# Optimization experiments

Measured on AMD Instinct MI355X. Metric: run time of the kernel, lower is better.

## Reference

```python
import jax, jax.numpy as jnp
import numpy as np

# module hyperparams (match init_kwargs)
C, K, S, RATIO, GC = 64, 7, 2, 2, 16
G = C // GC                      # 4 groups
KK = K * K                       # 49
NS = int(RATIO * S)              # 4
NN = NS * NS                     # 16
PAD = (K - 1) // 2               # 3
C1_IN = G * (2 * K * GC + KK)    # 1092
C1_OUT = G * NN * KK // 10       # 313
C2_OUT = G * NN * KK             # 3136
EPS = 1e-5


def _unfold(x, k, s, p):
    # torch.nn.Unfold: patches ordered (C, ki, kj) channel-major
    B, Cc, H, W = x.shape
    xp = jnp.pad(x, ((0, 0), (0, 0), (p, p), (p, p)))
    Ho = (H + 2 * p - k) // s + 1
    Wo = (W + 2 * p - k) // s + 1
    rows = jnp.arange(Ho)[:, None] * s + jnp.arange(k)[None, :]      # (Ho,k)
    cols = jnp.arange(Wo)[:, None] * s + jnp.arange(k)[None, :]      # (Wo,k)
    pat = xp[:, :, rows[:, :, None, None], cols[None, None, :, :]]   # (B,C,Ho,k,Wo,k)
    return pat.transpose(0, 1, 3, 5, 2, 4)                            # (B,C,k,k,Ho,Wo)


def setup_inputs() -> dict:
    key = jax.random.key(0)
    ks = jax.random.split(key, 5)
    x = jax.random.normal(ks[0], (8, C, 64, 64), dtype=jnp.float32)
    w1 = jax.random.normal(ks[1], (C1_OUT, C1_IN), dtype=jnp.float32) * 0.02
    gamma = jnp.ones((C1_OUT,), dtype=jnp.float32)   # BN weight (constant_init 1)
    beta = jnp.zeros((C1_OUT,), dtype=jnp.float32)   # BN bias
    w2 = jax.random.normal(ks[2], (C2_OUT, C1_OUT), dtype=jnp.float32) * 0.02
    b2 = jnp.zeros((C2_OUT,), dtype=jnp.float32)
    return {"x": x, "w1": w1, "gamma": gamma, "beta": beta, "w2": w2, "b2": b2}


def reference(x, w1, gamma, beta, w2, b2):
    B, _, H, W = x.shape
    pat = _unfold(x, K, S, PAD)                          # (B,C,K,K,Ho,Wo)
    Ho, Wo = pat.shape[-2], pat.shape[-1]
    xg = pat.reshape(B, G, GC, K, K, Ho, Wo)
    # three axis-wise max pools -> per-pixel descriptor
    x1 = xg.max(axis=2).reshape(B, G * K * K, Ho, Wo)
    x2 = xg.max(axis=3).reshape(B, G * GC * K, Ho, Wo)
    x3 = xg.max(axis=4).reshape(B, G * GC * K, Ho, Wo)
    feat = jnp.concatenate([x1, x2, x3], axis=1)         # (B, C1_IN, Ho, Wo)
    # conv1: 1x1 conv (no bias) + BN (batch stats) + ReLU
    h = jnp.einsum('bchw,oc->bohw', feat, w1)
    mu = h.mean(axis=(0, 2, 3), keepdims=True)
    var = h.var(axis=(0, 2, 3), keepdims=True)
    h = gamma[None, :, None, None] * (h - mu) * jax.lax.rsqrt(var + EPS) + beta[None, :, None, None]
    h = jax.nn.relu(h)
    # conv2: 1x1 conv with bias
    h2 = jnp.einsum('bchw,oc->bohw', h, w2) + b2[None, :, None, None]
    wt = h2.reshape(B, G, KK, NN, Ho, Wo)
    wt = jax.nn.softmax(wt, axis=2)                      # softmax over kernel positions
    # softmax-weighted patch reduction (mean over k*k)
    xk = xg.reshape(B, G, GC, KK, Ho, Wo)
    out = jnp.einsum('bgckhw,bgknhw->bgcnhw', xk, wt) / KK
    out = out.reshape(B, C, NS, NS, Ho, Wo)
    out = out.transpose(0, 1, 4, 2, 5, 3).reshape(B, C, Ho * NS, Wo * NS)
    return out
```

## Files before the change

kernel.cpp:

```cpp
#include <hip/hip_runtime.h>

namespace {
constexpr int kB    = 8;
constexpr int kC    = 64;
constexpr int kH    = 64, kW = 64;
constexpr int kNP   = 8192;
constexpr int kC1In = 1092;
constexpr int kKP   = 1152;
constexpr int kC1Out= 313;
constexpr int kC2Out= 3136;
constexpr int kC1P  = 320;
constexpr int kRowS = 56;
constexpr int kPosS = 16 * kRowS + 8;
constexpr int kPreFeat = 2048;
constexpr int kPreW2   = 490;
constexpr int kPreW1   = 1440;
constexpr int kPreBlocks = kPreFeat + kPreW2 + kPreW1;
}

typedef __attribute__((ext_vector_type(8))) short bf16x8;
typedef __attribute__((ext_vector_type(8))) _Float16 f16x8;
typedef __attribute__((ext_vector_type(2))) _Float16 h16x2;
typedef __attribute__((ext_vector_type(4))) float f32x4;

__device__ __forceinline__ unsigned short f2bf(float f) {
    unsigned u = __float_as_uint(f);
    unsigned r = (u + 0x7fffu + ((u >> 16) & 1u)) >> 16;
    return (unsigned short)r;
}

__global__ __launch_bounds__(256) void k_pre(const float* __restrict__ x,
        const float* __restrict__ w1, const float* __restrict__ w2,
        unsigned short* __restrict__ feat_bf, unsigned short* __restrict__ w1s,
        bf16x8* __restrict__ w2t, float* __restrict__ stats) {
    __shared__ float xs[16 * 7 * 40];
    int tid = threadIdx.x;
    int bid = blockIdx.x;

    if (bid < kPreFeat) {
        int g = bid >> 9, pt = bid & 511;
        int p0 = pt * 16;
        int b = p0 >> 10, i = (p0 >> 5) & 31, j0 = p0 & 31;
        int y0 = 2 * i - 3, xbase = 2 * j0 - 3;
        const float* xb = x + ((size_t)(b * 64 + g * 16) << 12);

        for (int idx = tid; idx < 16 * 7 * 40; idx += 256) {
            int ch = idx / 280, r2 = idx - ch * 280;
            int row = r2 / 40, col = r2 - row * 40;
            int yy = y0 + row, xx = xbase + col;
            float v = 0.f;
            if ((unsigned)yy < 64u && (unsigned)xx < 64u)
                v = xb[(ch << 12) + (yy << 6) + xx];
            xs[idx] = v;
        }
        __syncthreads();

        for (int o = tid; o < 16 * 273; o += 256) {
            int pos = o / 273, c = o - pos * 273;
            float m = -INFINITY;
            int cg;
            if (c < 49) {
                int a = c / 7, bk = c - a * 7;
                int base = a * 40 + 2 * pos + bk;
                #pragma unroll
                for (int ch = 0; ch < 16; ++ch) m = fmaxf(m, xs[ch * 280 + base]);
                cg = g * 49 + c;
            } else if (c < 161) {
                int r = c - 49;
                int ch = r / 7, bk = r - ch * 7;
                int base = ch * 280 + 2 * pos + bk;
                #pragma unroll
                for (int a = 0; a < 7; ++a) m = fmaxf(m, xs[base + a * 40]);
                cg = 196 + g * 112 + r;
            } else {
                int r = c - 161;
                int ch = r / 7, a = r - ch * 7;
                int base = ch * 280 + a * 40 + 2 * pos;
                #pragma unroll
                for (int bk = 0; bk < 7; ++bk) m = fmaxf(m, xs[base + bk]);
                cg = 644 + g * 112 + r;
            }
            feat_bf[(size_t)(p0 + pos) * kKP + cg] = f2bf(m);
        }
        if (g == 3) {
            for (int idx = tid; idx < 16 * 60; idx += 256) {
                int pos = idx / 60, c = idx - pos * 60;
                feat_bf[(size_t)(p0 + pos) * kKP + 1092 + c] = 0;
            }
        }
    } else if (bid < kPreFeat + kPreW2) {
        int idx = (bid - kPreFeat) * 256 + tid;
        int lane = idx & 63;
        int t = (idx >> 6) % 10;
        int k = (idx / 640) % 49;
        int g = idx / 31360;
        int n = lane & 15, c0 = t * 32 + ((lane >> 4) << 3);
        int row = g * 784 + k * 16 + n;
        bf16x8 hi;
        #pragma unroll
        for (int e = 0; e < 8; ++e) {
            int c = c0 + e;
            float v = (c < kC1Out) ? w2[(size_t)row * kC1Out + c] : 0.f;
            hi[e] = (short)f2bf(v);
        }
        w2t[idx] = hi;
    } else {
        int idx = (bid - kPreFeat - kPreW2) * 256 + tid;
        if (idx < 640) stats[idx] = 0.f;
        int r = idx / kKP, c = idx - r * kKP;
        float v = (r < kC1Out && c < kC1In) ? w1[(size_t)r * kC1In + c] : 0.f;
        w1s[idx] = f2bf(v);
    }
}

__global__ __launch_bounds__(512) void k_gemm1(
        const unsigned short* __restrict__ feat_bf, const unsigned short* __restrict__ w1s,
        float* __restrict__ h, float* __restrict__ sum_, float* __restrict__ sumsq_) {
    __shared__ unsigned short Ald[128 * 64];
    __shared__ unsigned short Bld[64 * 64];
    __shared__ float lsum[64], lsq[64];
    int tid = threadIdx.x;
    int lane = tid & 63, wv = tid >> 6;
    int row0 = blockIdx.x * 128, col0 = blockIdx.y * 64;
    int wr = wv >> 1, wc = wv & 1;
    int srow = lane >> 3;
    int soct = (lane & 7) ^ srow;
    int frow = lane & 15, fk = lane >> 4;

    f32x4 acc[2][2] = {};
    for (int k0 = 0; k0 < kKP; k0 += 64) {
        #pragma unroll
        for (int qq = 0; qq < 3; ++qq) {
            int q = wv + qq * 8;
            const unsigned short* srcbase;
            unsigned short* dst;
            int grow;
            if (q < 16) { grow = row0 + q * 8 + srow; srcbase = feat_bf; dst = Ald + q * 512; }
            else        { grow = col0 + (q - 16) * 8 + srow; srcbase = w1s; dst = Bld + (q - 16) * 512; }
            const unsigned short* src = srcbase + (size_t)grow * kKP + k0 + soct * 8;
            __builtin_amdgcn_global_load_lds(
                (const __attribute__((address_space(1))) unsigned int*)src,
                (__attribute__((address_space(3))) unsigned int*)dst, 16, 0, 0);
        }
        __syncthreads();
        #pragma unroll
        for (int ks = 0; ks < 2; ++ks) {
            int oct = ks * 4 + fk;
            bf16x8 a0, a1, b0, b1;
            { int r = wr * 32 + frow;      a0 = *(const bf16x8*)(Ald + (r * 8 + (oct ^ (r & 7))) * 8); }
            { int r = wr * 32 + 16 + frow; a1 = *(const bf16x8*)(Ald + (r * 8 + (oct ^ (r & 7))) * 8); }
            { int r = wc * 32 + frow;      b0 = *(const bf16x8*)(Bld + (r * 8 + (oct ^ (r & 7))) * 8); }
            { int r = wc * 32 + 16 + frow; b1 = *(const bf16x8*)(Bld + (r * 8 + (oct ^ (r & 7))) * 8); }
            acc[0][0] = __builtin_amdgcn_mfma_f32_16x16x32_bf16(a0, b0, acc[0][0], 0, 0, 0);
            acc[0][1] = __builtin_amdgcn_mfma_f32_16x16x32_bf16(a0, b1, acc[0][1], 0, 0, 0);
            acc[1][0] = __builtin_amdgcn_mfma_f32_16x16x32_bf16(a1, b0, acc[1][0], 0, 0, 0);
            acc[1][1] = __builtin_amdgcn_mfma_f32_16x16x32_bf16(a1, b1, acc[1][1], 0, 0, 0);
        }
        __syncthreads();
    }

    if (tid < 64) { lsum[tid] = 0.f; lsq[tid] = 0.f; }
    __syncthreads();
    #pragma unroll
    for (int i = 0; i < 2; ++i) {
        int mrow = row0 + wr * 32 + i * 16 + (lane >> 4) * 4;
        #pragma unroll
        for (int j = 0; j < 2; ++j) {
            int col_l = wc * 32 + j * 16 + (lane & 15);
            float s = 0.f, sq = 0.f;
            #pragma unroll
            for (int r = 0; r < 4; ++r) {
                float v = acc[i][j][r];
                h[(size_t)(mrow + r) * kC1P + col0 + col_l] = v;
                s += v; sq += v * v;
            }
            atomicAdd(&lsum[col_l], s);
            atomicAdd(&lsq[col_l], sq);
        }
    }
    __syncthreads();
    if (tid < 64 && col0 + tid < kC1Out) {
        atomicAdd(&sum_[col0 + tid], lsum[tid]);
        atomicAdd(&sumsq_[col0 + tid], lsq[tid]);
    }
}

__global__ void k_split_h(const float* __restrict__ h,
                          const float* __restrict__ sum_, const float* __restrict__ sumsq_,
                          const float* __restrict__ gamma, const float* __restrict__ beta,
                          bf16x8* __restrict__ ht_hi) {
    int idx = blockIdx.x * 256 + threadIdx.x;
    int lane = idx & 63;
    int t = (idx >> 6) % 10;
    int ptile = idx / 640;
    int pos = ptile * 16 + (lane & 15);
    int c0 = t * 32 + ((lane >> 4) << 3);
    float vv[8];
    *(float4*)&vv[0] = *(const float4*)(h + (size_t)pos * kC1P + c0);
    *(float4*)&vv[4] = *(const float4*)(h + (size_t)pos * kC1P + c0 + 4);
    bf16x8 hi;
    #pragma unroll
    for (int e = 0; e < 8; ++e) {
        int c = c0 + e;
        float v = 0.f;
        if (c < kC1Out) {
            float mu  = sum_[c]   * (1.f / kNP);
            float var = sumsq_[c] * (1.f / kNP) - mu * mu;
            float sc  = gamma[c] * rsqrtf(var + 1e-5f);
            float sh  = beta[c] - mu * sc;
            v = fmaxf(vv[e] * sc + sh, 0.f);
        }
        hi[e] = (short)f2bf(v);
    }
    ht_hi[idx] = hi;
}

__global__ __launch_bounds__(512) void k_fused(
        const bf16x8* __restrict__ ht_hi, const bf16x8* __restrict__ w2t,
        const float* __restrict__ b2, const float* __restrict__ x,
        float* __restrict__ out) {
    __shared__ _Float16 wtb[32 * kPosS];
    __shared__ float invt[512];
    __shared__ bf16x8 htl[1280];
    int tid = threadIdx.x;
    int lane = tid & 63, wv = tid >> 6;
    int bid = blockIdx.x;
    int g = bid >> 8, pt = bid & 255;

    {
        const bf16x8* hb = ht_hi + (size_t)(pt * 2) * 640;
        #pragma unroll
        for (int r = 0; r < 3; ++r) {
            int idx = r * 512 + tid;
            if (idx < 1280)
                __builtin_amdgcn_global_load_lds(
                    (const __attribute__((address_space(1))) unsigned int*)(hb + idx),
                    (__attribute__((address_space(3))) unsigned int*)(htl + idx), 16, 0, 0);
        }
    }
    __syncthreads();

    int col = lane & 15, rgrp = lane >> 4;
    for (int k = wv; k < 49; k += 16) {
        int k2 = k + 8;
        bool has2 = (k2 < 49);
        int k2c = has2 ? k2 : k;
        f32x4 acc00 = {0.f,0.f,0.f,0.f}, acc01 = {0.f,0.f,0.f,0.f};
        f32x4 acc10 = {0.f,0.f,0.f,0.f}, acc11 = {0.f,0.f,0.f,0.f};
        const bf16x8* wb0 = w2t + ((size_t)(g * 49 + k)   * 10) * 64 + lane;
        const bf16x8* wb1 = w2t + ((size_t)(g * 49 + k2c) * 10) * 64 + lane;
        bf16x8 bh0[10], bh1[10];
        #pragma unroll
        for (int t = 0; t < 10; ++t) { bh0[t] = wb0[t * 64]; bh1[t] = wb1[t * 64]; }
        #pragma unroll
        for (int t = 0; t < 10; ++t) {
            bf16x8 a0 = htl[t * 64 + lane];
            bf16x8 a1 = htl[640 + t * 64 + lane];
            acc00 = __builtin_amdgcn_mfma_f32_16x16x32_bf16(a0, bh0[t], acc00, 0, 0, 0);
            acc01 = __builtin_amdgcn_mfma_f32_16x16x32_bf16(a1, bh0[t], acc01, 0, 0, 0);
            acc10 = __builtin_amdgcn_mfma_f32_16x16x32_bf16(a0, bh1[t], acc10, 0, 0, 0);
            acc11 = __builtin_amdgcn_mfma_f32_16x16x32_bf16(a1, bh1[t], acc11, 0, 0, 0);
        }
        {
            float bias = b2[g * 784 + k * 16 + col];
            #pragma unroll
            for (int r = 0; r < 4; ++r) {
                int pos = rgrp * 4 + r;
                wtb[pos * kPosS + k * 16 + col]        = (_Float16)(acc00[r] + bias);
                wtb[(pos + 16) * kPosS + k * 16 + col] = (_Float16)(acc01[r] + bias);
            }
        }
        if (has2) {
            float bias = b2[g * 784 + k2 * 16 + col];
            #pragma unroll
            for (int r = 0; r < 4; ++r) {
                int pos = rgrp * 4 + r;
                wtb[pos * kPosS + k2 * 16 + col]        = (_Float16)(acc10[r] + bias);
                wtb[(pos + 16) * kPosS + k2 * 16 + col] = (_Float16)(acc11[r] + bias);
            }
        }
    }
    __syncthreads();

    {
        int pos = tid >> 4, n = tid & 15;
        const _Float16* baseA = wtb + pos * kPosS + n;
        f16x8 ee[7];
        float m = -INFINITY;
        #pragma unroll
        for (int c = 0; c < 7; ++c)
            #pragma unroll
            for (int e = 0; e < 8; ++e) {
                int k = c * 8 + e;
                if (k < 49) {
                    _Float16 v = baseA[k * 16];
                    ee[c][e] = v;
                    m = fmaxf(m, (float)v);
                } else ee[c][e] = (_Float16)0.f;
            }
        float s = 0.f;
        #pragma unroll
        for (int c = 0; c < 7; ++c)
            #pragma unroll
            for (int e = 0; e < 8; ++e) {
                int k = c * 8 + e;
                if (k < 49) {
                    float ex = __expf((float)ee[c][e] - m);
                    s += ex;
                    ee[c][e] = (_Float16)ex;
                }
            }
        __syncthreads();
        _Float16* baseB = wtb + pos * kPosS + n * kRowS;
        #pragma unroll
        for (int c = 0; c < 7; ++c) *(f16x8*)(baseB + c * 8) = ee[c];
        invt[tid] = 1.f / (s * 49.f);
    }
    __syncthreads();

    {
        int pos = tid & 31, c16 = tid >> 5;
        int p = pt * 32 + pos;
        int b = p >> 10, i = (p >> 5) & 31, j = p & 31;
        int y0 = 2 * i - 3, x0c = 2 * j - 3;
        const float* xc = x + (((size_t)b * 64 + g * 16 + c16) << 12);
        h16x2 patch2[28];
        #pragma unroll
        for (int a = 0; a < 7; ++a) {
            int yy = y0 + a;
            #pragma unroll
            for (int bk = 0; bk < 7; ++bk) {
                int kk = a * 7 + bk, xx = x0c + bk;
                float v = ((unsigned)yy < 64u && (unsigned)xx < 64u)
                        ? xc[(yy << 6) + xx] : 0.f;
                patch2[kk >> 1][kk & 1] = (_Float16)v;
            }
        }
        patch2[24][1] = (_Float16)0.f;
        patch2[25] = (h16x2)(_Float16)0.f;
        patch2[26] = (h16x2)(_Float16)0.f;
        patch2[27] = (h16x2)(_Float16)0.f;

        const _Float16* prow = wtb + pos * kPosS;
        float* outb = out + (((size_t)b * 64 + g * 16 + c16) << 14);
        #pragma unroll
        for (int n1 = 0; n1 < 4; ++n1) {
            f32x4 st;
            #pragma unroll
            for (int n2 = 0; n2 < 4; ++n2) {
                int n = n1 * 4 + n2;
                const f16x8* row = (const f16x8*)(prow + n * kRowS);
                float acc = 0.f;
                #pragma unroll
                for (int c = 0; c < 7; ++c) {
                    f16x8 w = row[c];
                    #pragma unroll
                    for (int q = 0; q < 4; ++q) {
                        h16x2 wp; wp[0] = w[2 * q]; wp[1] = w[2 * q + 1];
                        acc = __builtin_amdgcn_fdot2(patch2[c * 4 + q], wp, acc, false);
                    }
                }
                st[n2] = acc * invt[pos * 16 + n];
            }
            *(f32x4*)(outb + (i * 4 + n1) * 128 + j * 4) = st;
        }
    }
}

extern "C" void kernel_launch(void* const* d_in, const int* in_sizes, int n_in,
                              void* d_out, int out_size, void* d_ws, size_t ws_size,
                              hipStream_t stream) {
    const float* x     = (const float*)d_in[0];
    const float* w1    = (const float*)d_in[1];
    const float* gamma = (const float*)d_in[2];
    const float* beta  = (const float*)d_in[3];
    const float* w2    = (const float*)d_in[4];
    const float* b2    = (const float*)d_in[5];
    float* out = (float*)d_out;

    float* ws = (float*)d_ws;
    unsigned short* feat_bf = (unsigned short*)ws;
    float* h       = ws + 4718592;
    float* w2t_f   = h + 2621440;
    unsigned short* w1s = (unsigned short*)(w2t_f + 501760);
    float* sum_   = w2t_f + 501760 + 184320;
    float* sumsq_ = sum_ + 320;

    bf16x8* ht_hi = (bf16x8*)ws;
    bf16x8* w2t   = (bf16x8*)w2t_f;

    k_pre<<<kPreBlocks, 256, 0, stream>>>(x, w1, w2, feat_bf, w1s, w2t, sum_);
    k_gemm1<<<dim3(kNP / 128, 5), 512, 0, stream>>>(feat_bf, w1s, h, sum_, sumsq_);
    k_split_h<<<1280, 256, 0, stream>>>(h, sum_, sumsq_, gamma, beta, ht_hi);
    k_fused<<<1024, 512, 0, stream>>>(ht_hi, w2t, b2, x, out);
}
```

Before: 118.5 us.

## Fuse BN+ReLU split into fused kernel and store conv1 output as bf16

Removes the separate k_split_h kernel. Conv1 output is now written as bf16 instead of fp32, and the BatchNorm scale/shift, ReLU and fragment reordering are applied inside k_fused after staging h through shared memory. This drops one kernel launch and halves the h write/read traffic. In exchange, each of the 4 group blocks recomputes the normalization for the same tile, and h is rounded to bf16 before normalization rather than after, which adds some precision loss.

New measurement: 124.5 us. 1.05x slower.

```diff
diff --git a/kernel.cpp b/kernel.cpp
--- a/kernel.cpp
+++ b/kernel.cpp
@@ -12,6 +12,7 @@
 constexpr int kC1P  = 320;
 constexpr int kRowS = 56;
 constexpr int kPosS = 16 * kRowS + 8;
+constexpr int kHStS = 328;
 constexpr int kPreFeat = 2048;
 constexpr int kPreW2   = 490;
 constexpr int kPreW1   = 1440;
@@ -27,6 +28,9 @@
     unsigned u = __float_as_uint(f);
     unsigned r = (u + 0x7fffu + ((u >> 16) & 1u)) >> 16;
     return (unsigned short)r;
+}
+__device__ __forceinline__ float bf2f(unsigned short h) {
+    return __uint_as_float(((unsigned)h) << 16);
 }
 
 __global__ __launch_bounds__(256) void k_pre(const float* __restrict__ x,
@@ -115,7 +119,7 @@
 
 __global__ __launch_bounds__(512) void k_gemm1(
         const unsigned short* __restrict__ feat_bf, const unsigned short* __restrict__ w1s,
-        float* __restrict__ h, float* __restrict__ sum_, float* __restrict__ sumsq_) {
+        unsigned short* __restrict__ hb16, float* __restrict__ sum_, float* __restrict__ sumsq_) {
     __shared__ unsigned short Ald[128 * 64];
     __shared__ unsigned short Bld[64 * 64];
     __shared__ float lsum[64], lsq[64];
@@ -171,7 +175,7 @@
             #pragma unroll
             for (int r = 0; r < 4; ++r) {
                 float v = acc[i][j][r];
-                h[(size_t)(mrow + r) * kC1P + col0 + col_l] = v;
+                hb16[(size_t)(mrow + r) * kC1P + col0 + col_l] = f2bf(v);
                 s += v; sq += v * v;
             }
             atomicAdd(&lsum[col_l], s);
@@ -185,58 +189,55 @@
     }
 }
 
-__global__ void k_split_h(const float* __restrict__ h,
-                          const float* __restrict__ sum_, const float* __restrict__ sumsq_,
-                          const float* __restrict__ gamma, const float* __restrict__ beta,
-                          bf16x8* __restrict__ ht_hi) {
-    int idx = blockIdx.x * 256 + threadIdx.x;
-    int lane = idx & 63;
-    int t = (idx >> 6) % 10;
-    int ptile = idx / 640;
-    int pos = ptile * 16 + (lane & 15);
-    int c0 = t * 32 + ((lane >> 4) << 3);
-    float vv[8];
-    *(float4*)&vv[0] = *(const float4*)(h + (size_t)pos * kC1P + c0);
-    *(float4*)&vv[4] = *(const float4*)(h + (size_t)pos * kC1P + c0 + 4);
-    bf16x8 hi;
-    #pragma unroll
-    for (int e = 0; e < 8; ++e) {
-        int c = c0 + e;
-        float v = 0.f;
-        if (c < kC1Out) {
-            float mu  = sum_[c]   * (1.f / kNP);
-            float var = sumsq_[c] * (1.f / kNP) - mu * mu;
-            float sc  = gamma[c] * rsqrtf(var + 1e-5f);
-            float sh  = beta[c] - mu * sc;
-            v = fmaxf(vv[e] * sc + sh, 0.f);
-        }
-        hi[e] = (short)f2bf(v);
-    }
-    ht_hi[idx] = hi;
-}
-
 __global__ __launch_bounds__(512) void k_fused(
-        const bf16x8* __restrict__ ht_hi, const bf16x8* __restrict__ w2t,
-        const float* __restrict__ b2, const float* __restrict__ x,
-        float* __restrict__ out) {
+        const unsigned short* __restrict__ hb16,
+        const float* __restrict__ sum_, const float* __restrict__ sumsq_,
+        const float* __restrict__ gamma, const float* __restrict__ beta,
+        const bf16x8* __restrict__ w2t, const float* __restrict__ b2,
+        const float* __restrict__ x, float* __restrict__ out) {
     __shared__ _Float16 wtb[32 * kPosS];
     __shared__ float invt[512];
     __shared__ bf16x8 htl[1280];
+    unsigned short* hst = (unsigned short*)wtb;
+    float* scsh = (float*)(wtb + 11000);
     int tid = threadIdx.x;
     int lane = tid & 63, wv = tid >> 6;
     int bid = blockIdx.x;
     int g = bid >> 8, pt = bid & 255;
 
     {
-        const bf16x8* hb = ht_hi + (size_t)(pt * 2) * 640;
-        #pragma unroll
-        for (int r = 0; r < 3; ++r) {
-            int idx = r * 512 + tid;
-            if (idx < 1280)
-                __builtin_amdgcn_global_load_lds(
-                    (const __attribute__((address_space(1))) unsigned int*)(hb + idx),
-                    (__attribute__((address_space(3))) unsigned int*)(htl + idx), 16, 0, 0);
-        }
+        const unsigned short* hb = hb16 + (size_t)pt * 32 * kC1P;
+        for (int q = tid; q < 1280; q += 512) {
+            int pos = q / 40, off = q - pos * 40;
+            bf16x8 vfrag = *(const bf16x8*)(hb + pos * kC1P + off * 8);
+            *(bf16x8*)(hst + pos * kHStS + off * 8) = vfrag;
+        }
+        if (tid < 320) {
+            float mu  = sum_[tid]   * (1.f / kNP);
+            float var = sumsq_[tid] * (1.f / kNP) - mu * mu;
+            float sc  = (tid < kC1Out) ? gamma[tid] * rsqrtf(var + 1e-5f) : 0.f;
+            scsh[tid] = sc;
+            scsh[320 + tid] = (tid < kC1Out) ? beta[tid] - mu * sc : 0.f;
+        }
+    }
+    __syncthreads();
+
+    for (int v = tid; v < 1280; v += 512) {
+        int lv = v & 63;
+        int t = (v >> 6) % 10;
+        int half = v / 640;
+        int pos = half * 16 + (lv & 15);
+        int c0 = t * 32 + ((lv >> 4) << 3);
+        bf16x8 raw = *(const bf16x8*)(hst + pos * kHStS + c0);
+        bf16x8 hi;
+        #pragma unroll
+        for (int e = 0; e < 8; ++e) {
+            int c = c0 + e;
+            float f = bf2f((unsigned short)raw[e]);
+            float vo = (c < kC1Out) ? fmaxf(f * scsh[c] + scsh[320 + c], 0.f) : 0.f;
+            hi[e] = (short)f2bf(vo);
+        }
+        htl[v] = hi;
     }
     __syncthreads();
 
@@ -380,17 +381,15 @@
 
     float* ws = (float*)d_ws;
     unsigned short* feat_bf = (unsigned short*)ws;
-    float* h       = ws + 4718592;
-    float* w2t_f   = h + 2621440;
+    unsigned short* hb16 = (unsigned short*)(ws + 4718592);
+    float* w2t_f   = ws + 4718592 + 1310720;
     unsigned short* w1s = (unsigned short*)(w2t_f + 501760);
     float* sum_   = w2t_f + 501760 + 184320;
     float* sumsq_ = sum_ + 320;
 
-    bf16x8* ht_hi = (bf16x8*)ws;
-    bf16x8* w2t   = (bf16x8*)w2t_f;
+    bf16x8* w2t = (bf16x8*)w2t_f;
 
     k_pre<<<kPreBlocks, 256, 0, stream>>>(x, w1, w2, feat_bf, w1s, w2t, sum_);
-    k_gemm1<<<dim3(kNP / 128, 5), 512, 0, stream>>>(feat_bf, w1s, h, sum_, sumsq_);
-    k_split_h<<<1280, 256, 0, stream>>>(h, sum_, sumsq_, gamma, beta, ht_hi);
-    k_fused<<<1024, 512, 0, stream>>>(ht_hi, w2t, b2, x, out);
-}
+    k_gemm1<<<dim3(kNP / 128, 5), 512, 0, stream>>>(feat_bf, w1s, hb16, sum_, sumsq_);
+    k_fused<<<1024, 512, 0, stream>>>(hb16, sum_, sumsq_, gamma, beta, w2t, b2, x, out);
+}
```
